# Kernel optimization log

Hardware: AMD Instinct MI355X
Metric: run time of the kernel (lower is better)

Reference implementation:

```python
import jax, jax.numpy as jnp
import numpy as np

B, S, VOCAB, HID, NH, L, SPAN = 4, 512, 25, 512, 8, 12, 512
HEAD = HID // NH
FF = 4 * HID
EPS = 1e-7  # DebertaV2 layer_norm_eps


def _ln(x, g, b):
    m = x.mean(-1, keepdims=True)
    v = ((x - m) ** 2).mean(-1, keepdims=True)
    return (x - m) / jnp.sqrt(v + EPS) * g + b


def setup_inputs() -> dict:
    key = jax.random.key(0)
    ks = iter(jax.random.split(key, 16))
    w = lambda shape: jax.random.normal(next(ks), shape, jnp.float32) * 0.05
    return {
        "x": jax.random.randint(next(ks), (B, S), 0, VOCAB),
        "attention_mask": jnp.ones((B, S), jnp.int32),
        "word_emb": w((VOCAB, HID)),
        "emb_ln_g": jnp.ones((HID,), jnp.float32),
        "emb_ln_b": jnp.zeros((HID,), jnp.float32),
        "rel_emb": w((2 * SPAN, HID)),
        "Wq": w((L, HID, HID)), "bq": jnp.zeros((L, HID), jnp.float32),
        "Wk": w((L, HID, HID)), "bk": jnp.zeros((L, HID), jnp.float32),
        "Wv": w((L, HID, HID)), "bv": jnp.zeros((L, HID), jnp.float32),
        "Wpk": w((L, HID, HID)), "bpk": jnp.zeros((L, HID), jnp.float32),
        "Wpq": w((L, HID, HID)), "bpq": jnp.zeros((L, HID), jnp.float32),
        "Wo": w((L, HID, HID)), "bo": jnp.zeros((L, HID), jnp.float32),
        "ln1_g": jnp.ones((L, HID), jnp.float32), "ln1_b": jnp.zeros((L, HID), jnp.float32),
        "W1": w((L, HID, FF)), "b1": jnp.zeros((L, FF), jnp.float32),
        "W2": w((L, FF, HID)), "b2": jnp.zeros((L, HID), jnp.float32),
        "ln2_g": jnp.ones((L, HID), jnp.float32), "ln2_b": jnp.zeros((L, HID), jnp.float32),
        "cls_w": w((VOCAB, HID)), "cls_b": jnp.zeros((VOCAB,), jnp.float32),
    }


def _forward(x, attention_mask, word_emb, emb_ln_g, emb_ln_b, rel_emb,
             Wq, bq, Wk, bk, Wv, bv, Wpk, bpk, Wpq, bpq, Wo, bo,
             ln1_g, ln1_b, W1, b1, W2, b2, ln2_g, ln2_b, cls_w, cls_b):
    mask = attention_mask.astype(jnp.float32)
    # embeddings: word only (position_biased_input=False), LN, then masked
    h = _ln(word_emb[x], emb_ln_g, emb_ln_b) * mask[..., None]

    rel = jnp.arange(S)[:, None] - jnp.arange(S)[None, :]          # q_pos - k_pos
    c2p_idx = jnp.clip(rel + SPAN, 0, 2 * SPAN - 1)[None, None]    # [1,1,S,S]
    p2c_idx = jnp.clip(-rel + SPAN, 0, 2 * SPAN - 1)[None, None]
    attm = (mask[:, None, None, :] * mask[:, None, :, None]) > 0   # [B,1,S,S]
    scale = jnp.sqrt(jnp.float32(HEAD * 3))                        # scale_factor = 1 + len(pos_att_type)
    neg = jnp.finfo(jnp.float32).min

    def heads(t):  # [B,S,HID] -> [B,NH,S,HEAD]
        return t.reshape(B, S, NH, HEAD).transpose(0, 2, 1, 3)

    for l in range(L):
        q = heads(h @ Wq[l] + bq[l])
        k = heads(h @ Wk[l] + bk[l])
        v = heads(h @ Wv[l] + bv[l])
        # projected relative-position embeddings: [NH, 2*SPAN, HEAD]
        pk = (rel_emb @ Wpk[l] + bpk[l]).reshape(2 * SPAN, NH, HEAD).transpose(1, 0, 2)
        pq = (rel_emb @ Wpq[l] + bpq[l]).reshape(2 * SPAN, NH, HEAD).transpose(1, 0, 2)

        scores = jnp.einsum('bhqd,bhkd->bhqk', q, k)
        # c2p: query content vs key position, gathered at clamp(rel+span)
        c2p = jnp.take_along_axis(jnp.einsum('bhqd,hpd->bhqp', q, pk), c2p_idx, axis=-1)
        # p2c: key content vs query position, gathered at clamp(-rel+span) then transposed
        p2c = jnp.take_along_axis(jnp.einsum('bhkd,hpd->bhkp', k, pq), p2c_idx, axis=-1)
        scores = (scores + c2p + jnp.swapaxes(p2c, -1, -2)) / scale

        scores = jnp.where(attm, scores, neg)
        probs = jnp.where(attm, jax.nn.softmax(scores, axis=-1), 0.0)  # XSoftmax
        ctx = jnp.einsum('bhqk,bhkd->bhqd', probs, v).transpose(0, 2, 1, 3).reshape(B, S, HID)
        h = _ln(ctx @ Wo[l] + bo[l] + h, ln1_g[l], ln1_b[l])
        f = jax.nn.gelu(h @ W1[l] + b1[l], approximate=False) @ W2[l] + b2[l]
        h = _ln(f + h, ln2_g[l], ln2_b[l])

    logits = h @ cls_w.T + cls_b
    return h, logits


def reference(x, attention_mask, word_emb, emb_ln_g, emb_ln_b, rel_emb,
              Wq, bq, Wk, bk, Wv, bv, Wpk, bpk, Wpq, bpq, Wo, bo,
              ln1_g, ln1_b, W1, b1, W2, b2, ln2_g, ln2_b, cls_w, cls_b):
    return _forward(x, attention_mask, word_emb, emb_ln_g, emb_ln_b, rel_emb,
                    Wq, bq, Wk, bk, Wv, bv, Wpk, bpk, Wpq, bpq, Wo, bo,
                    ln1_g, ln1_b, W1, b1, W2, b2, ln2_g, ln2_b, cls_w, cls_b)
```

## Files before the change

kernel.cpp:

```cpp
#include <hip/hip_runtime.h>
#include <hip/hip_bf16.h>

#define BATCH  4
#define SEQ    512
#define TOK    (BATCH*SEQ)
#define HID    512
#define NHEAD  8
#define HEAD   64
#define FFDIM  2048
#define NLAYER 12
#define SPAN2  1024
#define VOCAB  25
#define LNEPS  1e-7f
#define NEG_BIG -3.0e38f

typedef __attribute__((ext_vector_type(8))) short bf16x8;
typedef __attribute__((ext_vector_type(4))) float floatx4;

#define MFMA16(a, b, c) __builtin_amdgcn_mfma_f32_16x16x32_bf16((a), (b), (c), 0, 0, 0)

__device__ __forceinline__ float b2f(unsigned short u) {
    return __uint_as_float(((unsigned int)u) << 16);
}
__device__ __forceinline__ unsigned short f2b(float f) {
    __hip_bfloat16 h = __float2bfloat16(f);
    return *(unsigned short*)&h;
}

__device__ __forceinline__ float block_reduce_sum(float v, float* red) {
    int tid = threadIdx.x;
    red[tid] = v; __syncthreads();
    for (int s = 128; s > 0; s >>= 1) { if (tid < s) red[tid] += red[tid + s]; __syncthreads(); }
    float r = red[0]; __syncthreads();
    return r;
}

__global__ void embed_ln_kernel(const int* __restrict__ x, const int* __restrict__ am,
                                const float* __restrict__ word_emb,
                                const float* __restrict__ g, const float* __restrict__ bb,
                                float* __restrict__ h, unsigned short* __restrict__ hb) {
    __shared__ float red[256];
    int t = blockIdx.x, tid = threadIdx.x;
    const float* we = word_emb + (size_t)x[t] * HID;
    float v1 = we[tid], v2 = we[tid + 256];
    float mean = block_reduce_sum(v1 + v2, red) * (1.0f / HID);
    float d1 = v1 - mean, d2 = v2 - mean;
    float var = block_reduce_sum(d1 * d1 + d2 * d2, red) * (1.0f / HID);
    float rstd = rsqrtf(var + LNEPS);
    float maskf = (float)am[t];
    size_t base = (size_t)t * HID;
    float o1 = (d1 * rstd * g[tid]       + bb[tid])       * maskf;
    float o2 = (d2 * rstd * g[tid + 256] + bb[tid + 256]) * maskf;
    h[base + tid] = o1;        h[base + tid + 256] = o2;
    hb[base + tid] = f2b(o1);  hb[base + tid + 256] = f2b(o2);
}

__global__ void add_ln_kernel(const float* __restrict__ tmp,
                              const float* __restrict__ g, const float* __restrict__ bb,
                              float* __restrict__ h, unsigned short* __restrict__ hb) {
    __shared__ float red[256];
    int t = blockIdx.x, tid = threadIdx.x;
    size_t base = (size_t)t * HID;
    float v1 = tmp[base + tid] + h[base + tid];
    float v2 = tmp[base + tid + 256] + h[base + tid + 256];
    float mean = block_reduce_sum(v1 + v2, red) * (1.0f / HID);
    float d1 = v1 - mean, d2 = v2 - mean;
    float var = block_reduce_sum(d1 * d1 + d2 * d2, red) * (1.0f / HID);
    float rstd = rsqrtf(var + LNEPS);
    float o1 = d1 * rstd * g[tid]       + bb[tid];
    float o2 = d2 * rstd * g[tid + 256] + bb[tid + 256];
    h[base + tid] = o1;        h[base + tid + 256] = o2;
    hb[base + tid] = f2b(o1);  hb[base + tid + 256] = f2b(o2);
}

__global__ void add_ln2_kernel(const float* __restrict__ t1a, const float* __restrict__ t1b,
                               const float* __restrict__ g, const float* __restrict__ bb,
                               float* __restrict__ h, unsigned short* __restrict__ hb) {
    __shared__ float red[256];
    int t = blockIdx.x, tid = threadIdx.x;
    size_t base = (size_t)t * HID;
    float v1 = t1a[base + tid] + t1b[base + tid] + h[base + tid];
    float v2 = t1a[base + tid + 256] + t1b[base + tid + 256] + h[base + tid + 256];
    float mean = block_reduce_sum(v1 + v2, red) * (1.0f / HID);
    float d1 = v1 - mean, d2 = v2 - mean;
    float var = block_reduce_sum(d1 * d1 + d2 * d2, red) * (1.0f / HID);
    float rstd = rsqrtf(var + LNEPS);
    float o1 = d1 * rstd * g[tid]       + bb[tid];
    float o2 = d2 * rstd * g[tid + 256] + bb[tid + 256];
    h[base + tid] = o1;        h[base + tid + 256] = o2;
    hb[base + tid] = f2b(o1);  hb[base + tid + 256] = f2b(o2);
}

__global__ void cvt_rel_kernel(const float* __restrict__ in, unsigned short* __restrict__ out) {
    int i = (blockIdx.x * 256 + threadIdx.x) * 4;
    float4 v = *(const float4*)(in + i);
    out[i] = f2b(v.x); out[i+1] = f2b(v.y); out[i+2] = f2b(v.z); out[i+3] = f2b(v.w);
}

__global__ void tcvt_kernel(const float* __restrict__ in, unsigned short* __restrict__ out,
                            int K, int N) {
    __shared__ float tile[32][33];
    int l = blockIdx.z;
    const float* ip = in + (size_t)l * K * N;
    unsigned short* op = out + (size_t)l * K * N;
    int kb = blockIdx.y * 32, nb = blockIdx.x * 32;
    int tx = threadIdx.x, ty = threadIdx.y;
    #pragma unroll
    for (int i = 0; i < 32; i += 8) tile[ty + i][tx] = ip[(size_t)(kb + ty + i) * N + nb + tx];
    __syncthreads();
    #pragma unroll
    for (int i = 0; i < 32; i += 8) op[(size_t)(nb + ty + i) * K + kb + tx] = f2b(tile[tx][ty + i]);
}

__global__ void tcvt6_kernel(const float* __restrict__ Wq, const float* __restrict__ Wk,
                             const float* __restrict__ Wv, const float* __restrict__ Wpk,
                             const float* __restrict__ Wpq, const float* __restrict__ Wo,
                             unsigned short* __restrict__ out) {
    __shared__ float tile[32][33];
    int z = blockIdx.z, l = z / 6, w = z - l * 6;
    const float* src = w == 0 ? Wq : w == 1 ? Wk : w == 2 ? Wv : w == 3 ? Wpk : w == 4 ? Wpq : Wo;
    const float* ip = src + (size_t)l * HID * HID;
    unsigned short* op = out + ((size_t)w * NLAYER + l) * HID * HID;
    int kb = blockIdx.y * 32, nb = blockIdx.x * 32;
    int tx = threadIdx.x, ty = threadIdx.y;
    #pragma unroll
    for (int i = 0; i < 32; i += 8) tile[ty + i][tx] = ip[(size_t)(kb + ty + i) * HID + nb + tx];
    __syncthreads();
    #pragma unroll
    for (int i = 0; i < 32; i += 8) op[(size_t)(nb + ty + i) * HID + kb + tx] = f2b(tile[tx][ty + i]);
}

__device__ __forceinline__ void gemm_tile_bt(
    const unsigned short* __restrict__ A, const unsigned short* __restrict__ Bt,
    int row0, int col0, int K, int kbeg, int kend,
    floatx4 (&acc)[2][2], unsigned short (&As)[64][72], unsigned short (&Bs)[64][72]) {
    int tid = threadIdx.x;
    int lane = tid & 63, wid = tid >> 6;
    int wm = wid >> 1, wn = wid & 1;
    int m16 = lane & 15, quad = lane >> 4;
    int sr = tid >> 2, sc = (tid & 3) << 4;
    const unsigned short* Ag = A + (size_t)(row0 + sr) * K + sc;
    const unsigned short* Bg = Bt + (size_t)(col0 + sr) * K + sc;
    for (int k0 = kbeg; k0 < kend; k0 += 64) {
        uint4 av0 = *(const uint4*)(Ag + k0);
        uint4 av1 = *(const uint4*)(Ag + k0 + 8);
        uint4 bv0 = *(const uint4*)(Bg + k0);
        uint4 bv1 = *(const uint4*)(Bg + k0 + 8);
        *(uint4*)&As[sr][sc]     = av0;
        *(uint4*)&As[sr][sc + 8] = av1;
        *(uint4*)&Bs[sr][sc]     = bv0;
        *(uint4*)&Bs[sr][sc + 8] = bv1;
        __syncthreads();
        #pragma unroll
        for (int kk = 0; kk < 2; kk++) {
            bf16x8 a0 = *(const bf16x8*)&As[wm * 32 + m16][kk * 32 + quad * 8];
            bf16x8 a1 = *(const bf16x8*)&As[wm * 32 + 16 + m16][kk * 32 + quad * 8];
            bf16x8 b0 = *(const bf16x8*)&Bs[wn * 32 + m16][kk * 32 + quad * 8];
            bf16x8 b1 = *(const bf16x8*)&Bs[wn * 32 + 16 + m16][kk * 32 + quad * 8];
            acc[0][0] = MFMA16(a0, b0, acc[0][0]);
            acc[0][1] = MFMA16(a0, b1, acc[0][1]);
            acc[1][0] = MFMA16(a1, b0, acc[1][0]);
            acc[1][1] = MFMA16(a1, b1, acc[1][1]);
        }
        __syncthreads();
    }
}

template<bool OUT_BF16, bool GELU, int SPLITK>
__global__ __launch_bounds__(256) void gemm_bt(
    const unsigned short* __restrict__ A, const unsigned short* __restrict__ Bt,
    const float* __restrict__ bias, void* __restrict__ Cp, int N, int K) {
    __shared__ unsigned short As[64][72], Bs[64][72];
    int row0 = blockIdx.y * 64, col0 = blockIdx.x * 64;
    int kseg = K / SPLITK;
    int kbeg = kseg * blockIdx.z, kend = kbeg + kseg;
    floatx4 acc[2][2];
    #pragma unroll
    for (int mi = 0; mi < 2; mi++)
        #pragma unroll
        for (int ni = 0; ni < 2; ni++) acc[mi][ni] = (floatx4){0.f, 0.f, 0.f, 0.f};
    gemm_tile_bt(A, Bt, row0, col0, K, kbeg, kend, acc, As, Bs);

    int tid = threadIdx.x, lane = tid & 63, wid = tid >> 6;
    int wm = wid >> 1, wn = wid & 1, m16 = lane & 15, quad = lane >> 4;
    size_t outoff = (size_t)blockIdx.z * (size_t)(gridDim.y << 6) * N;
    #pragma unroll
    for (int ni = 0; ni < 2; ni++) {
        int colg = col0 + wn * 32 + ni * 16 + m16;
        float bval = (SPLITK == 1 || blockIdx.z == 0) ? bias[colg] : 0.0f;
        #pragma unroll
        for (int mi = 0; mi < 2; mi++) {
            #pragma unroll
            for (int r = 0; r < 4; r++) {
                int rowg = row0 + wm * 32 + mi * 16 + quad * 4 + r;
                float v = acc[mi][ni][r] + bval;
                if (GELU) v = 0.5f * v * (1.0f + erff(v * 0.70710678118654752f));
                if (OUT_BF16) ((unsigned short*)Cp)[(size_t)rowg * N + colg] = f2b(v);
                else          ((float*)Cp)[outoff + (size_t)rowg * N + colg] = v;
            }
        }
    }
}

__global__ __launch_bounds__(256) void qkvp_gemm(
    const unsigned short* __restrict__ hb, const unsigned short* __restrict__ relb,
    const unsigned short* __restrict__ Wqt, const unsigned short* __restrict__ Wkt,
    const unsigned short* __restrict__ Wvt, const unsigned short* __restrict__ Wpkt,
    const unsigned short* __restrict__ Wpqt,
    const float* __restrict__ bq, const float* __restrict__ bk, const float* __restrict__ bv,
    const float* __restrict__ bpk, const float* __restrict__ bpq,
    unsigned short* __restrict__ qb, unsigned short* __restrict__ kb,
    unsigned short* __restrict__ vb, unsigned short* __restrict__ pkb,
    unsigned short* __restrict__ pqb) {
    __shared__ unsigned short As[64][72], Bs[64][72];
    int bid = blockIdx.x;
    int xcd = bid & 7, slot = bid >> 3;
    int op, j;
    if (xcd < 6) { op = xcd >> 1; j = slot * 2 + (xcd & 1); }
    else         { op = xcd - 3;  j = slot; }
    int trow = j >> 3, tcol = j & 7;
    const unsigned short* A; const unsigned short* Bt; const float* bias; unsigned short* C;
    if (op < 3) {
        A = hb;
        Bt   = op == 0 ? Wqt : op == 1 ? Wkt : Wvt;
        bias = op == 0 ? bq  : op == 1 ? bk  : bv;
        C    = op == 0 ? qb  : op == 1 ? kb  : vb;
    } else {
        A = relb;
        Bt   = op == 3 ? Wpkt : Wpqt;
        bias = op == 3 ? bpk  : bpq;
        C    = op == 3 ? pkb  : pqb;
    }
    floatx4 acc[2][2];
    #pragma unroll
    for (int mi = 0; mi < 2; mi++)
        #pragma unroll
        for (int ni = 0; ni < 2; ni++) acc[mi][ni] = (floatx4){0.f, 0.f, 0.f, 0.f};
    gemm_tile_bt(A, Bt, trow * 64, tcol * 64, HID, 0, HID, acc, As, Bs);

    int tid = threadIdx.x, lane = tid & 63, wid = tid >> 6;
    int wm = wid >> 1, wn = wid & 1, m16 = lane & 15, quad = lane >> 4;
    #pragma unroll
    for (int ni = 0; ni < 2; ni++) {
        int colg = tcol * 64 + wn * 32 + ni * 16 + m16;
        float bval = bias[colg];
        #pragma unroll
        for (int mi = 0; mi < 2; mi++) {
            #pragma unroll
            for (int r = 0; r < 4; r++) {
                int rowg = trow * 64 + wm * 32 + mi * 16 + quad * 4 + r;
                C[(size_t)rowg * HID + colg] = f2b(acc[mi][ni][r] + bval);
            }
        }
    }
}

template<bool OUT_BF16, bool GELU>
__global__ __launch_bounds__(256) void mfma_gemm(
    const unsigned short* __restrict__ A, const float* __restrict__ B,
    const float* __restrict__ bias, void* __restrict__ Cp, int N, int K) {
    __shared__ unsigned short As[64][72];
    __shared__ unsigned short Bs[64][72];
    int tid = threadIdx.x;
    int lane = tid & 63, wid = tid >> 6;
    int wm = wid >> 1, wn = wid & 1;
    int row0 = blockIdx.y * 64, col0 = blockIdx.x * 64;
    int m16 = lane & 15, quad = lane >> 4;

    int ar = tid >> 2, ac = (tid & 3) << 4;
    int bk = (tid >> 3) << 1, bn = (tid & 7) << 3;

    const unsigned short* Ag = A + (size_t)(row0 + ar) * K + ac;
    const float* Bg = B + (size_t)bk * N + col0 + bn;

    floatx4 acc[2][2];
    #pragma unroll
    for (int mi = 0; mi < 2; mi++)
        #pragma unroll
        for (int ni = 0; ni < 2; ni++) acc[mi][ni] = (floatx4){0.f, 0.f, 0.f, 0.f};

    for (int k0 = 0; k0 < K; k0 += 64) {
        uint4 av0 = *(const uint4*)(Ag + k0);
        uint4 av1 = *(const uint4*)(Ag + k0 + 8);
        const float* br0 = Bg + (size_t)k0 * N;
        const float* br1 = br0 + N;
        float4 b00 = *(const float4*)br0, b01 = *(const float4*)(br0 + 4);
        float4 b10 = *(const float4*)br1, b11 = *(const float4*)(br1 + 4);
        *(uint4*)&As[ar][ac] = av0;
        *(uint4*)&As[ar][ac + 8] = av1;
        float lo[8] = {b00.x, b00.y, b00.z, b00.w, b01.x, b01.y, b01.z, b01.w};
        float hi[8] = {b10.x, b10.y, b10.z, b10.w, b11.x, b11.y, b11.z, b11.w};
        #pragma unroll
        for (int i = 0; i < 8; i++) {
            unsigned int p = (unsigned int)f2b(lo[i]) | ((unsigned int)f2b(hi[i]) << 16);
            *(unsigned int*)&Bs[bn + i][bk] = p;
        }
        __syncthreads();
        #pragma unroll
        for (int kk = 0; kk < 2; kk++) {
            bf16x8 a0 = *(const bf16x8*)&As[wm * 32 + m16][kk * 32 + quad * 8];
            bf16x8 a1 = *(const bf16x8*)&As[wm * 32 + 16 + m16][kk * 32 + quad * 8];
            bf16x8 b0 = *(const bf16x8*)&Bs[wn * 32 + m16][kk * 32 + quad * 8];
            bf16x8 b1 = *(const bf16x8*)&Bs[wn * 32 + 16 + m16][kk * 32 + quad * 8];
            acc[0][0] = MFMA16(a0, b0, acc[0][0]);
            acc[0][1] = MFMA16(a0, b1, acc[0][1]);
            acc[1][0] = MFMA16(a1, b0, acc[1][0]);
            acc[1][1] = MFMA16(a1, b1, acc[1][1]);
        }
        __syncthreads();
    }
    #pragma unroll
    for (int ni = 0; ni < 2; ni++) {
        int colg = col0 + wn * 32 + ni * 16 + m16;
        float bv = bias[colg];
        #pragma unroll
        for (int mi = 0; mi < 2; mi++) {
            #pragma unroll
            for (int r = 0; r < 4; r++) {
                int rowg = row0 + wm * 32 + mi * 16 + quad * 4 + r;
                float v = acc[mi][ni][r] + bv;
                if (GELU) v = 0.5f * v * (1.0f + erff(v * 0.70710678118654752f));
                if (OUT_BF16) ((unsigned short*)Cp)[(size_t)rowg * N + colg] = f2b(v);
                else          ((float*)Cp)[(size_t)rowg * N + colg] = v;
            }
        }
    }
}

__global__ __launch_bounds__(256, 2) void attn_kernel(
    const unsigned short* __restrict__ Q, const unsigned short* __restrict__ K,
    const unsigned short* __restrict__ V,
    const unsigned short* __restrict__ PK, const unsigned short* __restrict__ PQ,
    const int* __restrict__ am, unsigned short* __restrict__ ctx) {
    __shared__ unsigned short Ks[2][32][72];
    __shared__ unsigned short Vt[2][64][40];
    __shared__ float Afs[4][16][49];
    __shared__ float Bfs[4][32][50];
    __shared__ unsigned short Pls[4][16][40];
    __shared__ int mkk[2][32];
    __shared__ float mergeML[2][2][16];

    int bid = blockIdx.x;
    int hh = bid & 7;
    int b  = (bid >> 3) & 3;
    int q0 = (bid >> 5) * 32;
    int tid = threadIdx.x;
    int lane = tid & 63, wave = tid >> 6;
    int u = wave >> 1;
    int s = wave & 1;
    int quad = lane >> 4, m16 = lane & 15;
    const float inv_scale = 0.07216878364870323f;

    const unsigned short* qg = Q + (size_t)(b * SEQ + q0 + u * 16 + m16) * HID + hh * HEAD;
    bf16x8 qf0 = *(const bf16x8*)(qg + quad * 8);
    bf16x8 qf1 = *(const bf16x8*)(qg + 32 + quad * 8);

    int sr = tid >> 3;
    int sc = (tid & 7) * 8;
    int vkey = ((sc >> 3) & 3) << 3;

    floatx4 accO[4];
    #pragma unroll
    for (int nt = 0; nt < 4; nt++) accO[nt] = (floatx4){0.f, 0.f, 0.f, 0.f};
    float mreg[4] = {NEG_BIG, NEG_BIG, NEG_BIG, NEG_BIG};
    float lreg[4] = {0.f, 0.f, 0.f, 0.f};

    for (int ph = 0; ph < 8; ph++) {
        int t = 2 * ph + s;
        int P0  = q0 - 32 * t + 481;
        int P20 = 32 * t - q0 + 481;
        int Jb  = 16 - 16 * u;

        bf16x8 pkf[3][2], pqf[3][2];
        #pragma unroll
        for (int nt = 0; nt < 3; nt++) {
            int prow = P0 + 16 * u + nt * 16 + m16;
            const unsigned short* pg = PK + (size_t)prow * HID + hh * HEAD + quad * 8;
            pkf[nt][0] = *(const bf16x8*)pg;
            pkf[nt][1] = *(const bf16x8*)(pg + 32);
            int prow2 = P20 + Jb + nt * 16 + m16;
            if (prow2 > 1023) prow2 = 1023;
            const unsigned short* pg2 = PQ + (size_t)prow2 * HID + hh * HEAD + quad * 8;
            pqf[nt][0] = *(const bf16x8*)pg2;
            pqf[nt][1] = *(const bf16x8*)(pg2 + 32);
        }

        #pragma unroll
        for (int sl = 0; sl < 2; sl++) {
            int k0 = ph * 64 + sl * 32;
            const unsigned short* kg = K + (size_t)(b * SEQ + k0 + sr) * HID + hh * HEAD + sc;
            *(uint4*)&Ks[sl][sr][sc] = *(const uint4*)kg;
            uint4 vv = *(const uint4*)(V + (size_t)(b * SEQ + k0 + sr) * HID + hh * HEAD + sc);
            unsigned short* vp = (unsigned short*)&vv;
            #pragma unroll
            for (int j = 0; j < 8; j++) Vt[sl][sc + j][sr ^ vkey] = vp[j];
        }
        if (tid < 64) mkk[tid >> 5][tid & 31] = am[b * SEQ + ph * 64 + tid];
        __syncthreads();

        floatx4 accS[2];
        accS[0] = (floatx4){0.f, 0.f, 0.f, 0.f};
        accS[1] = (floatx4){0.f, 0.f, 0.f, 0.f};
        #pragma unroll
        for (int n = 0; n < 2; n++) {
            bf16x8 kfa = *(const bf16x8*)&Ks[s][n * 16 + m16][quad * 8];
            bf16x8 kfb = *(const bf16x8*)&Ks[s][n * 16 + m16][32 + quad * 8];
            accS[n] = MFMA16(qf0, kfa, accS[n]);
            accS[n] = MFMA16(qf1, kfb, accS[n]);
        }

        {
            floatx4 accA[3];
            #pragma unroll
            for (int nt = 0; nt < 3; nt++) {
                accA[nt] = (floatx4){0.f, 0.f, 0.f, 0.f};
                accA[nt] = MFMA16(qf0, pkf[nt][0], accA[nt]);
                accA[nt] = MFMA16(qf1, pkf[nt][1], accA[nt]);
            }
            #pragma unroll
            for (int nt = 0; nt < 3; nt++)
                #pragma unroll
                for (int r = 0; r < 4; r++)
                    Afs[wave][quad * 4 + r][nt * 16 + m16] = accA[nt][r];
        }

        {
            floatx4 accB[2][3];
            #pragma unroll
            for (int mt = 0; mt < 2; mt++) {
                bf16x8 afa = *(const bf16x8*)&Ks[s][mt * 16 + m16][quad * 8];
                bf16x8 afb = *(const bf16x8*)&Ks[s][mt * 16 + m16][32 + quad * 8];
                #pragma unroll
                for (int nt = 0; nt < 3; nt++) {
                    accB[mt][nt] = (floatx4){0.f, 0.f, 0.f, 0.f};
                    accB[mt][nt] = MFMA16(afa, pqf[nt][0], accB[mt][nt]);
                    accB[mt][nt] = MFMA16(afb, pqf[nt][1], accB[mt][nt]);
                }
            }
            #pragma unroll
            for (int mt = 0; mt < 2; mt++)
                #pragma unroll
                for (int nt = 0; nt < 3; nt++)
                    #pragma unroll
                    for (int r = 0; r < 4; r++)
                        Bfs[wave][mt * 16 + quad * 4 + r][nt * 16 + m16] = accB[mt][nt][r];
        }

        float sv[2][4];
        float tmax[4] = {NEG_BIG, NEG_BIG, NEG_BIG, NEG_BIG};
        #pragma unroll
        for (int n = 0; n < 2; n++) {
            #pragma unroll
            for (int r = 0; r < 4; r++) {
                int qq = quad * 4 + r;
                int kc = n * 16 + m16;
                float av = Afs[wave][qq][qq - kc + 31];
                float bv = Bfs[wave][kc][kc - qq + 15];
                float x = (accS[n][r] + av + bv) * inv_scale;
                x = mkk[s][kc] ? x : NEG_BIG;
                sv[n][r] = x;
                tmax[r] = fmaxf(tmax[r], x);
            }
        }
        float alpha[4], psum[4];
        #pragma unroll
        for (int r = 0; r < 4; r++) {
            float tm = tmax[r];
            tm = fmaxf(tm, __shfl_xor(tm, 1));
            tm = fmaxf(tm, __shfl_xor(tm, 2));
            tm = fmaxf(tm, __shfl_xor(tm, 4));
            tm = fmaxf(tm, __shfl_xor(tm, 8));
            float mo = mreg[r];
            float mn = fmaxf(mo, tm);
            alpha[r] = __expf(mo - mn);
            mreg[r] = mn;
        }
        #pragma unroll
        for (int r = 0; r < 4; r++) psum[r] = 0.f;
        #pragma unroll
        for (int n = 0; n < 2; n++) {
            #pragma unroll
            for (int r = 0; r < 4; r++) {
                float p = (sv[n][r] > -1.5e38f) ? __expf(sv[n][r] - mreg[r]) : 0.0f;
                unsigned short pb = f2b(p);
                Pls[wave][quad * 4 + r][n * 16 + m16] = pb;
                psum[r] += b2f(pb);
            }
        }
        #pragma unroll
        for (int r = 0; r < 4; r++) {
            float ps = psum[r];
            ps += __shfl_xor(ps, 1);
            ps += __shfl_xor(ps, 2);
            ps += __shfl_xor(ps, 4);
            ps += __shfl_xor(ps, 8);
            lreg[r] = lreg[r] * alpha[r] + ps;
        }
        #pragma unroll
        for (int nt = 0; nt < 4; nt++)
            #pragma unroll
            for (int r = 0; r < 4; r++) accO[nt][r] *= alpha[r];
        {
            bf16x8 pf = *(const bf16x8*)&Pls[wave][m16][quad * 8];
            #pragma unroll
            for (int nt = 0; nt < 4; nt++) {
                int d = nt * 16 + m16;
                int kq = (quad ^ ((d >> 3) & 3)) * 8;
                bf16x8 vf = *(const bf16x8*)&Vt[s][d][kq];
                accO[nt] = MFMA16(pf, vf, accO[nt]);
            }
        }
        __syncthreads();
    }

    __syncthreads();
    float* mo = &Bfs[0][0][0];
    if (s == 1) {
        #pragma unroll
        for (int nt = 0; nt < 4; nt++)
            #pragma unroll
            for (int r = 0; r < 4; r++)
                mo[u * 1056 + (quad * 4 + r) * 66 + nt * 16 + m16] = accO[nt][r];
        if (m16 == 0) {
            #pragma unroll
            for (int r = 0; r < 4; r++) {
                mergeML[u][0][quad * 4 + r] = mreg[r];
                mergeML[u][1][quad * 4 + r] = lreg[r];
            }
        }
    }
    __syncthreads();
    if (s == 0) {
        #pragma unroll
        for (int r = 0; r < 4; r++) {
            int row = quad * 4 + r;
            float m1 = mergeML[u][0][row], l1 = mergeML[u][1][row];
            float m0 = mreg[r], l0 = lreg[r];
            float mt = fmaxf(m0, m1);
            float a0 = __expf(m0 - mt), a1 = __expf(m1 - mt);
            float lt = l0 * a0 + l1 * a1;
            float inv = lt > 0.0f ? 1.0f / lt : 0.0f;
            inv *= (float)am[b * SEQ + q0 + u * 16 + row];
            #pragma unroll
            for (int nt = 0; nt < 4; nt++) {
                float o1 = mo[u * 1056 + row * 66 + nt * 16 + m16];
                float val = (accO[nt][r] * a0 + o1 * a1) * inv;
                ctx[(size_t)(b * SEQ + q0 + u * 16 + row) * HID + hh * HEAD + nt * 16 + m16] = f2b(val);
            }
        }
    }
}

__global__ void copy_f_kernel(const float* __restrict__ in, float* __restrict__ out, int n) {
    int i = blockIdx.x * 256 + threadIdx.x;
    if (i < n) out[i] = in[i];
}
__global__ void cls_kernel(const float* __restrict__ h, const float* __restrict__ cls_w,
                           const float* __restrict__ cls_b, float* __restrict__ out) {
    int t = blockIdx.x, v = threadIdx.x;
    if (v < VOCAB) {
        const float* hr = h + (size_t)t * HID;
        const float* wr = cls_w + (size_t)v * HID;
        float acc = cls_b[v];
        for (int d = 0; d < HID; d++) acc += hr[d] * wr[d];
        out[t * VOCAB + v] = acc;
    }
}

extern "C" void kernel_launch(void* const* d_in, const int* in_sizes, int n_in,
                              void* d_out, int out_size, void* d_ws, size_t ws_size,
                              hipStream_t stream) {
    const int* x     = (const int*)d_in[0];
    const int* am    = (const int*)d_in[1];
    const float* word_emb = (const float*)d_in[2];
    const float* emb_g    = (const float*)d_in[3];
    const float* emb_b    = (const float*)d_in[4];
    const float* rel_emb  = (const float*)d_in[5];
    const float* Wq  = (const float*)d_in[6];  const float* bq  = (const float*)d_in[7];
    const float* Wk  = (const float*)d_in[8];  const float* bk  = (const float*)d_in[9];
    const float* Wv  = (const float*)d_in[10]; const float* bv  = (const float*)d_in[11];
    const float* Wpk = (const float*)d_in[12]; const float* bpk = (const float*)d_in[13];
    const float* Wpq = (const float*)d_in[14]; const float* bpq = (const float*)d_in[15];
    const float* Wo  = (const float*)d_in[16]; const float* bo  = (const float*)d_in[17];
    const float* ln1g = (const float*)d_in[18]; const float* ln1b = (const float*)d_in[19];
    const float* W1  = (const float*)d_in[20]; const float* b1  = (const float*)d_in[21];
    const float* W2  = (const float*)d_in[22]; const float* b2  = (const float*)d_in[23];
    const float* ln2g = (const float*)d_in[24]; const float* ln2b = (const float*)d_in[25];
    const float* cls_w = (const float*)d_in[26]; const float* cls_b = (const float*)d_in[27];

    char* wsb = (char*)d_ws;
    const size_t NEED_BIG = 107u << 20;

    if (ws_size >= NEED_BIG) {
        float* h  = (float*)wsb;
        float* t1 = (float*)(wsb + (4u << 20));
        float* t2 = (float*)(wsb + (8u << 20));
        unsigned short* qb   = (unsigned short*)(wsb + (12u << 20));
        unsigned short* kb   = (unsigned short*)(wsb + (14u << 20));
        unsigned short* vb   = (unsigned short*)(wsb + (16u << 20));
        unsigned short* pkb  = (unsigned short*)(wsb + (18u << 20));
        unsigned short* pqb  = (unsigned short*)(wsb + (19u << 20));
        unsigned short* relb = (unsigned short*)(wsb + (20u << 20));
        unsigned short* hb   = (unsigned short*)(wsb + (21u << 20));
        unsigned short* ctx  = hb;
        unsigned short* ffb  = qb;
        unsigned short* Wqt  = (unsigned short*)(wsb + (23u << 20));
        unsigned short* W1t  = (unsigned short*)(wsb + (59u << 20));
        unsigned short* W2t  = (unsigned short*)(wsb + (83u << 20));

        const size_t M512 = (size_t)HID * HID;

        tcvt6_kernel<<<dim3(16, 16, 72), dim3(32, 8), 0, stream>>>(Wq, Wk, Wv, Wpk, Wpq, Wo, Wqt);
        tcvt_kernel<<<dim3(64, 16, 12), dim3(32, 8), 0, stream>>>(W1, W1t, HID, FFDIM);
        tcvt_kernel<<<dim3(16, 64, 12), dim3(32, 8), 0, stream>>>(W2, W2t, FFDIM, HID);
        cvt_rel_kernel<<<dim3(SPAN2 * HID / 1024), dim3(256), 0, stream>>>(rel_emb, relb);
        embed_ln_kernel<<<dim3(TOK), dim3(256), 0, stream>>>(x, am, word_emb, emb_g, emb_b, h, hb);

        for (int l = 0; l < NLAYER; l++) {
            qkvp_gemm<<<dim3(1024), dim3(256), 0, stream>>>(
                hb, relb,
                Wqt + (size_t)(0 * NLAYER + l) * M512, Wqt + (size_t)(1 * NLAYER + l) * M512,
                Wqt + (size_t)(2 * NLAYER + l) * M512, Wqt + (size_t)(3 * NLAYER + l) * M512,
                Wqt + (size_t)(4 * NLAYER + l) * M512,
                bq + l * HID, bk + l * HID, bv + l * HID, bpk + l * HID, bpq + l * HID,
                qb, kb, vb, pkb, pqb);

            attn_kernel<<<dim3(512), dim3(256), 0, stream>>>(
                qb, kb, vb, pkb, pqb, am, ctx);

            gemm_bt<false, false, 2><<<dim3(HID / 64, TOK / 64, 2), dim3(256), 0, stream>>>(
                ctx, Wqt + (size_t)(5 * NLAYER + l) * M512, bo + l * HID, t1, HID, HID);
            add_ln2_kernel<<<dim3(TOK), dim3(256), 0, stream>>>(t1, t2, ln1g + l * HID, ln1b + l * HID, h, hb);

            gemm_bt<true, true, 1><<<dim3(FFDIM / 64, TOK / 64, 1), dim3(256), 0, stream>>>(
                hb, W1t + (size_t)l * HID * FFDIM, b1 + l * FFDIM, ffb, FFDIM, HID);
            gemm_bt<false, false, 2><<<dim3(HID / 64, TOK / 64, 2), dim3(256), 0, stream>>>(
                ffb, W2t + (size_t)l * HID * FFDIM, b2 + l * HID, t1, HID, FFDIM);
            add_ln2_kernel<<<dim3(TOK), dim3(256), 0, stream>>>(t1, t2, ln2g + l * HID, ln2b + l * HID, h, hb);
        }

        float* out_f = (float*)d_out;
        copy_f_kernel<<<dim3(TOK * HID / 256), dim3(256), 0, stream>>>(h, out_f, TOK * HID);
        cls_kernel<<<dim3(TOK), dim3(32), 0, stream>>>(h, cls_w, cls_b, out_f + TOK * HID);
        return;
    }

    const size_t NEEDED = 19u << 20;
    if (ws_size < NEEDED) return;
    float* h  = (float*)wsb;
    float* t1 = (float*)(wsb + (4u << 20));
    unsigned short* qb   = (unsigned short*)(wsb + (8u << 20));
    unsigned short* kb   = qb  + (1u << 20);
    unsigned short* vb   = kb  + (1u << 20);
    unsigned short* pkb  = vb  + (1u << 20);
    unsigned short* pqb  = pkb + (1u << 19);
    unsigned short* relb = (unsigned short*)(wsb + (16u << 20));
    unsigned short* hb   = (unsigned short*)(wsb + (17u << 20));
    unsigned short* ctx  = hb;
    unsigned short* ffb  = qb;

    cvt_rel_kernel<<<dim3(SPAN2 * HID / 1024), dim3(256), 0, stream>>>(rel_emb, relb);
    embed_ln_kernel<<<dim3(TOK), dim3(256), 0, stream>>>(x, am, word_emb, emb_g, emb_b, h, hb);

    for (int l = 0; l < NLAYER; l++) {
        const float* Wq_l = Wq + (size_t)l * HID * HID;
        const float* Wk_l = Wk + (size_t)l * HID * HID;
        const float* Wv_l = Wv + (size_t)l * HID * HID;
        const float* Wo_l = Wo + (size_t)l * HID * HID;
        const float* Wpk_l = Wpk + (size_t)l * HID * HID;
        const float* Wpq_l = Wpq + (size_t)l * HID * HID;
        const float* W1_l = W1 + (size_t)l * HID * FFDIM;
        const float* W2_l = W2 + (size_t)l * FFDIM * HID;

        mfma_gemm<true,  false><<<dim3(HID/64, TOK/64),   dim3(256), 0, stream>>>(hb,   Wq_l,  bq + l*HID,  qb,  HID, HID);
        mfma_gemm<true,  false><<<dim3(HID/64, TOK/64),   dim3(256), 0, stream>>>(hb,   Wk_l,  bk + l*HID,  kb,  HID, HID);
        mfma_gemm<true,  false><<<dim3(HID/64, TOK/64),   dim3(256), 0, stream>>>(hb,   Wv_l,  bv + l*HID,  vb,  HID, HID);
        mfma_gemm<true,  false><<<dim3(HID/64, SPAN2/64), dim3(256), 0, stream>>>(relb, Wpk_l, bpk + l*HID, pkb, HID, HID);
        mfma_gemm<true,  false><<<dim3(HID/64, SPAN2/64), dim3(256), 0, stream>>>(relb, Wpq_l, bpq + l*HID, pqb, HID, HID);

        attn_kernel<<<dim3(512), dim3(256), 0, stream>>>(qb, kb, vb, pkb, pqb, am, ctx);

        mfma_gemm<false, false><<<dim3(HID/64, TOK/64),   dim3(256), 0, stream>>>(ctx,  Wo_l,  bo + l*HID,  t1,  HID, HID);
        add_ln_kernel<<<dim3(TOK), dim3(256), 0, stream>>>(t1, ln1g + l*HID, ln1b + l*HID, h, hb);

        mfma_gemm<true,  true ><<<dim3(FFDIM/64, TOK/64), dim3(256), 0, stream>>>(hb,   W1_l,  b1 + l*FFDIM, ffb, FFDIM, HID);
        mfma_gemm<false, false><<<dim3(HID/64, TOK/64),   dim3(256), 0, stream>>>(ffb,  W2_l,  b2 + l*HID,  t1,  HID, FFDIM);
        add_ln_kernel<<<dim3(TOK), dim3(256), 0, stream>>>(t1, ln2g + l*HID, ln2b + l*HID, h, hb);
    }

    float* out_f = (float*)d_out;
    copy_f_kernel<<<dim3(TOK*HID/256), dim3(256), 0, stream>>>(h, out_f, TOK*HID);
    cls_kernel<<<dim3(TOK), dim3(32), 0, stream>>>(h, cls_w, cls_b, out_f + TOK*HID);
}
```

Measured before the change: 1.460 ms.

## Pre-transpose V and double-buffer K/PK/PQ fragments in registers in attention

The attention kernel no longer stages K and transposed V tiles through shared memory with block-wide barriers. It loads K, PK and PQ fragments straight into registers, ping-ponging two register sets so the next phase's loads overlap the current phase's MFMAs, and it reads V from a layout already transposed per (batch, head). The mask is packed into a per-lane bitmask once up front. To feed this, V is transposed in the fused-QKV epilogue (op==2) and a separate vtr_kernel is added on the default path, which costs extra launches, memory traffic, workspace, and more register pressure under launch_bounds(256,2).

After: 1.505 ms. +3.0%, slower.

```diff
diff --git a/kernel.cpp b/kernel.cpp
--- a/kernel.cpp
+++ b/kernel.cpp
@@ -128,6 +128,22 @@
     __syncthreads();
     #pragma unroll
     for (int i = 0; i < 32; i += 8) op[(size_t)(nb + ty + i) * HID + kb + tx] = f2b(tile[tx][ty + i]);
+}
+
+__global__ void vtr_kernel(const unsigned short* __restrict__ in, unsigned short* __restrict__ out) {
+    __shared__ unsigned short tile[32][33];
+    int tb = blockIdx.y * 32, cb = blockIdx.x * 32;
+    int tx = threadIdx.x, ty = threadIdx.y;
+    #pragma unroll
+    for (int i = 0; i < 32; i += 8)
+        tile[ty + i][tx] = in[(size_t)(tb + ty + i) * HID + cb + tx];
+    __syncthreads();
+    int bq = tb >> 9, sq = tb & 511;
+    #pragma unroll
+    for (int i = 0; i < 32; i += 8) {
+        int c = cb + ty + i;
+        out[((size_t)(bq * NHEAD + (c >> 6)) * HEAD + (c & 63)) * SEQ + sq + tx] = tile[tx][ty + i];
+    }
 }
 
 __device__ __forceinline__ void gemm_tile_bt(
@@ -240,16 +256,36 @@
 
     int tid = threadIdx.x, lane = tid & 63, wid = tid >> 6;
     int wm = wid >> 1, wn = wid & 1, m16 = lane & 15, quad = lane >> 4;
-    #pragma unroll
-    for (int ni = 0; ni < 2; ni++) {
-        int colg = tcol * 64 + wn * 32 + ni * 16 + m16;
-        float bval = bias[colg];
-        #pragma unroll
-        for (int mi = 0; mi < 2; mi++) {
-            #pragma unroll
-            for (int r = 0; r < 4; r++) {
-                int rowg = trow * 64 + wm * 32 + mi * 16 + quad * 4 + r;
-                C[(size_t)rowg * HID + colg] = f2b(acc[mi][ni][r] + bval);
+    if (op == 2) {
+        #pragma unroll
+        for (int ni = 0; ni < 2; ni++) {
+            int colg = tcol * 64 + wn * 32 + ni * 16 + m16;
+            float bval = bias[colg];
+            int h2 = colg >> 6, d2 = colg & 63;
+            #pragma unroll
+            for (int mi = 0; mi < 2; mi++) {
+                int rg0 = trow * 64 + wm * 32 + mi * 16 + quad * 4;
+                int b2 = rg0 >> 9, sq0 = rg0 & 511;
+                ushort4 pv;
+                pv.x = f2b(acc[mi][ni][0] + bval);
+                pv.y = f2b(acc[mi][ni][1] + bval);
+                pv.z = f2b(acc[mi][ni][2] + bval);
+                pv.w = f2b(acc[mi][ni][3] + bval);
+                *(ushort4*)(C + ((size_t)(b2 * NHEAD + h2) * HEAD + d2) * SEQ + sq0) = pv;
+            }
+        }
+    } else {
+        #pragma unroll
+        for (int ni = 0; ni < 2; ni++) {
+            int colg = tcol * 64 + wn * 32 + ni * 16 + m16;
+            float bval = bias[colg];
+            #pragma unroll
+            for (int mi = 0; mi < 2; mi++) {
+                #pragma unroll
+                for (int r = 0; r < 4; r++) {
+                    int rowg = trow * 64 + wm * 32 + mi * 16 + quad * 4 + r;
+                    C[(size_t)rowg * HID + colg] = f2b(acc[mi][ni][r] + bval);
+                }
             }
         }
     }
@@ -329,21 +365,19 @@
 
 __global__ __launch_bounds__(256, 2) void attn_kernel(
     const unsigned short* __restrict__ Q, const unsigned short* __restrict__ K,
-    const unsigned short* __restrict__ V,
+    const unsigned short* __restrict__ Vtg,
     const unsigned short* __restrict__ PK, const unsigned short* __restrict__ PQ,
     const int* __restrict__ am, unsigned short* __restrict__ ctx) {
-    __shared__ unsigned short Ks[2][32][72];
-    __shared__ unsigned short Vt[2][64][40];
     __shared__ float Afs[4][16][49];
     __shared__ float Bfs[4][32][50];
     __shared__ unsigned short Pls[4][16][40];
-    __shared__ int mkk[2][32];
     __shared__ float mergeML[2][2][16];
 
     int bid = blockIdx.x;
     int hh = bid & 7;
     int b  = (bid >> 3) & 3;
     int q0 = (bid >> 5) * 32;
+    int bh = b * NHEAD + hh;
     int tid = threadIdx.x;
     int lane = tid & 63, wave = tid >> 6;
     int u = wave >> 1;
@@ -355,9 +389,10 @@
     bf16x8 qf0 = *(const bf16x8*)(qg + quad * 8);
     bf16x8 qf1 = *(const bf16x8*)(qg + 32 + quad * 8);
 
-    int sr = tid >> 3;
-    int sc = (tid & 7) * 8;
-    int vkey = ((sc >> 3) & 3) << 3;
+    unsigned int mbits = 0;
+    #pragma unroll
+    for (int i = 0; i < 32; i++)
+        mbits |= (unsigned int)(am[b * SEQ + i * 16 + m16] != 0) << i;
 
     floatx4 accO[4];
     #pragma unroll
@@ -365,57 +400,51 @@
     float mreg[4] = {NEG_BIG, NEG_BIG, NEG_BIG, NEG_BIG};
     float lreg[4] = {0.f, 0.f, 0.f, 0.f};
 
-    for (int ph = 0; ph < 8; ph++) {
-        int t = 2 * ph + s;
-        int P0  = q0 - 32 * t + 481;
-        int P20 = 32 * t - q0 + 481;
-        int Jb  = 16 - 16 * u;
-
-        bf16x8 pkf[3][2], pqf[3][2];
+    struct KPRegs { bf16x8 kf[2][2]; bf16x8 pk[3][2]; bf16x8 pq[3][2]; };
+
+    auto load_kp = [&](int t, KPRegs& R) {
+        const unsigned short* kg = K + (size_t)(b * SEQ + t * 32 + m16) * HID + hh * HEAD + quad * 8;
+        #pragma unroll
+        for (int n = 0; n < 2; n++) {
+            R.kf[n][0] = *(const bf16x8*)(kg + n * 16 * HID);
+            R.kf[n][1] = *(const bf16x8*)(kg + n * 16 * HID + 32);
+        }
+        int baseA = q0 + 16 * u - 32 * t + 481;
+        const unsigned short* pg = PK + (size_t)(baseA + m16) * HID + hh * HEAD + quad * 8;
         #pragma unroll
         for (int nt = 0; nt < 3; nt++) {
-            int prow = P0 + 16 * u + nt * 16 + m16;
-            const unsigned short* pg = PK + (size_t)prow * HID + hh * HEAD + quad * 8;
-            pkf[nt][0] = *(const bf16x8*)pg;
-            pkf[nt][1] = *(const bf16x8*)(pg + 32);
-            int prow2 = P20 + Jb + nt * 16 + m16;
-            if (prow2 > 1023) prow2 = 1023;
-            const unsigned short* pg2 = PQ + (size_t)prow2 * HID + hh * HEAD + quad * 8;
-            pqf[nt][0] = *(const bf16x8*)pg2;
-            pqf[nt][1] = *(const bf16x8*)(pg2 + 32);
-        }
-
-        #pragma unroll
-        for (int sl = 0; sl < 2; sl++) {
-            int k0 = ph * 64 + sl * 32;
-            const unsigned short* kg = K + (size_t)(b * SEQ + k0 + sr) * HID + hh * HEAD + sc;
-            *(uint4*)&Ks[sl][sr][sc] = *(const uint4*)kg;
-            uint4 vv = *(const uint4*)(V + (size_t)(b * SEQ + k0 + sr) * HID + hh * HEAD + sc);
-            unsigned short* vp = (unsigned short*)&vv;
-            #pragma unroll
-            for (int j = 0; j < 8; j++) Vt[sl][sc + j][sr ^ vkey] = vp[j];
-        }
-        if (tid < 64) mkk[tid >> 5][tid & 31] = am[b * SEQ + ph * 64 + tid];
-        __syncthreads();
+            R.pk[nt][0] = *(const bf16x8*)(pg + nt * 16 * HID);
+            R.pk[nt][1] = *(const bf16x8*)(pg + nt * 16 * HID + 32);
+        }
+        int baseB = 32 * t - q0 - 16 * u + 497;
+        const unsigned short* pg2 = PQ + (size_t)(baseB + m16) * HID + hh * HEAD + quad * 8;
+        #pragma unroll
+        for (int nt = 0; nt < 3; nt++) {
+            R.pq[nt][0] = *(const bf16x8*)(pg2 + nt * 16 * HID);
+            R.pq[nt][1] = *(const bf16x8*)(pg2 + nt * 16 * HID + 32);
+        }
+    };
+
+    auto do_phase = [&](int t, KPRegs& R) {
+        bf16x8 vf[4];
+        const unsigned short* vg = Vtg + ((size_t)bh * HEAD + m16) * SEQ + t * 32 + quad * 8;
+        #pragma unroll
+        for (int nt = 0; nt < 4; nt++) vf[nt] = *(const bf16x8*)(vg + nt * 16 * SEQ);
 
         floatx4 accS[2];
-        accS[0] = (floatx4){0.f, 0.f, 0.f, 0.f};
-        accS[1] = (floatx4){0.f, 0.f, 0.f, 0.f};
         #pragma unroll
         for (int n = 0; n < 2; n++) {
-            bf16x8 kfa = *(const bf16x8*)&Ks[s][n * 16 + m16][quad * 8];
-            bf16x8 kfb = *(const bf16x8*)&Ks[s][n * 16 + m16][32 + quad * 8];
-            accS[n] = MFMA16(qf0, kfa, accS[n]);
-            accS[n] = MFMA16(qf1, kfb, accS[n]);
-        }
-
+            accS[n] = (floatx4){0.f, 0.f, 0.f, 0.f};
+            accS[n] = MFMA16(qf0, R.kf[n][0], accS[n]);
+            accS[n] = MFMA16(qf1, R.kf[n][1], accS[n]);
+        }
         {
             floatx4 accA[3];
             #pragma unroll
             for (int nt = 0; nt < 3; nt++) {
                 accA[nt] = (floatx4){0.f, 0.f, 0.f, 0.f};
-                accA[nt] = MFMA16(qf0, pkf[nt][0], accA[nt]);
-                accA[nt] = MFMA16(qf1, pkf[nt][1], accA[nt]);
+                accA[nt] = MFMA16(qf0, R.pk[nt][0], accA[nt]);
+                accA[nt] = MFMA16(qf1, R.pk[nt][1], accA[nt]);
             }
             #pragma unroll
             for (int nt = 0; nt < 3; nt++)
@@ -423,20 +452,16 @@
                 for (int r = 0; r < 4; r++)
                     Afs[wave][quad * 4 + r][nt * 16 + m16] = accA[nt][r];
         }
-
         {
             floatx4 accB[2][3];
             #pragma unroll
-            for (int mt = 0; mt < 2; mt++) {
-                bf16x8 afa = *(const bf16x8*)&Ks[s][mt * 16 + m16][quad * 8];
-                bf16x8 afb = *(const bf16x8*)&Ks[s][mt * 16 + m16][32 + quad * 8];
+            for (int mt = 0; mt < 2; mt++)
                 #pragma unroll
                 for (int nt = 0; nt < 3; nt++) {
                     accB[mt][nt] = (floatx4){0.f, 0.f, 0.f, 0.f};
-                    accB[mt][nt] = MFMA16(afa, pqf[nt][0], accB[mt][nt]);
-                    accB[mt][nt] = MFMA16(afb, pqf[nt][1], accB[mt][nt]);
+                    accB[mt][nt] = MFMA16(R.kf[mt][0], R.pq[nt][0], accB[mt][nt]);
+                    accB[mt][nt] = MFMA16(R.kf[mt][1], R.pq[nt][1], accB[mt][nt]);
                 }
-            }
             #pragma unroll
             for (int mt = 0; mt < 2; mt++)
                 #pragma unroll
@@ -445,7 +470,7 @@
                     for (int r = 0; r < 4; r++)
                         Bfs[wave][mt * 16 + quad * 4 + r][nt * 16 + m16] = accB[mt][nt][r];
         }
-
+        unsigned int bm = mbits >> (2 * t);
         float sv[2][4];
         float tmax[4] = {NEG_BIG, NEG_BIG, NEG_BIG, NEG_BIG};
         #pragma unroll
@@ -457,12 +482,12 @@
                 float av = Afs[wave][qq][qq - kc + 31];
                 float bv = Bfs[wave][kc][kc - qq + 15];
                 float x = (accS[n][r] + av + bv) * inv_scale;
-                x = mkk[s][kc] ? x : NEG_BIG;
+                x = ((bm >> n) & 1) ? x : NEG_BIG;
                 sv[n][r] = x;
                 tmax[r] = fmaxf(tmax[r], x);
             }
         }
-        float alpha[4], psum[4];
+        float alpha[4];
         #pragma unroll
         for (int r = 0; r < 4; r++) {
             float tm = tmax[r];
@@ -475,8 +500,7 @@
             alpha[r] = __expf(mo - mn);
             mreg[r] = mn;
         }
-        #pragma unroll
-        for (int r = 0; r < 4; r++) psum[r] = 0.f;
+        float psum[4] = {0.f, 0.f, 0.f, 0.f};
         #pragma unroll
         for (int n = 0; n < 2; n++) {
             #pragma unroll
@@ -503,24 +527,28 @@
         {
             bf16x8 pf = *(const bf16x8*)&Pls[wave][m16][quad * 8];
             #pragma unroll
-            for (int nt = 0; nt < 4; nt++) {
-                int d = nt * 16 + m16;
-                int kq = (quad ^ ((d >> 3) & 3)) * 8;
-                bf16x8 vf = *(const bf16x8*)&Vt[s][d][kq];
-                accO[nt] = MFMA16(pf, vf, accO[nt]);
-            }
-        }
-        __syncthreads();
-    }
-
-    __syncthreads();
-    float* mo = &Bfs[0][0][0];
+            for (int nt = 0; nt < 4; nt++)
+                accO[nt] = MFMA16(pf, vf[nt], accO[nt]);
+        }
+    };
+
+    KPRegs Ra, Rb;
+    load_kp(s, Ra);
+    for (int pp = 0; pp < 4; pp++) {
+        int t0 = 4 * pp + s;
+        load_kp(t0 + 2, Rb);
+        do_phase(t0, Ra);
+        if (pp < 3) load_kp(t0 + 4, Ra);
+        do_phase(t0 + 2, Rb);
+    }
+
+    float* mo = &Bfs[u * 2 + 1][0][0];
     if (s == 1) {
         #pragma unroll
         for (int nt = 0; nt < 4; nt++)
             #pragma unroll
             for (int r = 0; r < 4; r++)
-                mo[u * 1056 + (quad * 4 + r) * 66 + nt * 16 + m16] = accO[nt][r];
+                mo[(quad * 4 + r) * 66 + nt * 16 + m16] = accO[nt][r];
         if (m16 == 0) {
             #pragma unroll
             for (int r = 0; r < 4; r++) {
@@ -543,7 +571,7 @@
             inv *= (float)am[b * SEQ + q0 + u * 16 + row];
             #pragma unroll
             for (int nt = 0; nt < 4; nt++) {
-                float o1 = mo[u * 1056 + row * 66 + nt * 16 + m16];
+                float o1 = mo[row * 66 + nt * 16 + m16];
                 float val = (accO[nt][r] * a0 + o1 * a1) * inv;
                 ctx[(size_t)(b * SEQ + q0 + u * 16 + row) * HID + hh * HEAD + nt * 16 + m16] = f2b(val);
             }
@@ -645,7 +673,7 @@
         return;
     }
 
-    const size_t NEEDED = 19u << 20;
+    const size_t NEEDED = 21u << 20;
     if (ws_size < NEEDED) return;
     float* h  = (float*)wsb;
     float* t1 = (float*)(wsb + (4u << 20));
@@ -656,6 +684,7 @@
     unsigned short* pqb  = pkb + (1u << 19);
     unsigned short* relb = (unsigned short*)(wsb + (16u << 20));
     unsigned short* hb   = (unsigned short*)(wsb + (17u << 20));
+    unsigned short* vbt  = (unsigned short*)(wsb + (19u << 20));
     unsigned short* ctx  = hb;
     unsigned short* ffb  = qb;
 
@@ -675,10 +704,11 @@
         mfma_gemm<true,  false><<<dim3(HID/64, TOK/64),   dim3(256), 0, stream>>>(hb,   Wq_l,  bq + l*HID,  qb,  HID, HID);
         mfma_gemm<true,  false><<<dim3(HID/64, TOK/64),   dim3(256), 0, stream>>>(hb,   Wk_l,  bk + l*HID,  kb,  HID, HID);
         mfma_gemm<true,  false><<<dim3(HID/64, TOK/64),   dim3(256), 0, stream>>>(hb,   Wv_l,  bv + l*HID,  vb,  HID, HID);
+        vtr_kernel<<<dim3(HID/32, TOK/32), dim3(32, 8), 0, stream>>>(vb, vbt);
         mfma_gemm<true,  false><<<dim3(HID/64, SPAN2/64), dim3(256), 0, stream>>>(relb, Wpk_l, bpk + l*HID, pkb, HID, HID);
         mfma_gemm<true,  false><<<dim3(HID/64, SPAN2/64), dim3(256), 0, stream>>>(relb, Wpq_l, bpq + l*HID, pqb, HID, HID);
 
-        attn_kernel<<<dim3(512), dim3(256), 0, stream>>>(qb, kb, vb, pkb, pqb, am, ctx);
+        attn_kernel<<<dim3(512), dim3(256), 0, stream>>>(qb, kb, vbt, pkb, pqb, am, ctx);
 
         mfma_gemm<false, false><<<dim3(HID/64, TOK/64),   dim3(256), 0, stream>>>(ctx,  Wo_l,  bo + l*HID,  t1,  HID, HID);
         add_ln_kernel<<<dim3(TOK), dim3(256), 0, stream>>>(t1, ln1g + l*HID, ln1b + l*HID, h, hb);
```
